# Kernel optimization log

Hardware: AMD Instinct MI355X
Metric: run time of the kernel (lower is better)

## Reference

```python
import jax, jax.numpy as jnp
import numpy as np

HEADS = 8
DIM_HEAD = 64
ROPE_THETA = 10000.0


def _rope(t):
    # t: [b, h, n, d]; interleaved-pair rotation as in rotary-embedding-torch
    n, d = t.shape[-2], t.shape[-1]
    inv_freq = 1.0 / (ROPE_THETA ** (jnp.arange(0, d, 2, dtype=jnp.float32) / d))  # [d/2]
    freqs = jnp.arange(n, dtype=jnp.float32)[:, None] * inv_freq[None, :]  # [n, d/2]
    freqs = jnp.repeat(freqs, 2, axis=-1)  # [n, d], repeated per pair
    cos, sin = jnp.cos(freqs), jnp.sin(freqs)
    x1 = t[..., 0::2]
    x2 = t[..., 1::2]
    rot = jnp.stack((-x2, x1), axis=-1).reshape(t.shape)  # rotate_half
    return t * cos + rot * sin


def setup_inputs() -> dict:
    key = jax.random.key(0)
    k1, k2, k3, k4 = jax.random.split(key, 4)
    b, n, dim = 2, 2048, 512
    hidden = HEADS * DIM_HEAD
    x = jax.random.normal(k1, (b, n, dim), dtype=jnp.float32)
    pos_bias = jax.random.normal(k2, (HEADS, n, n), dtype=jnp.float32) * 0.02
    w_qkv = jax.random.normal(k3, (dim, 3 * hidden), dtype=jnp.float32) * (dim ** -0.5)
    w_out = jax.random.normal(k4, (hidden, dim), dtype=jnp.float32) * (hidden ** -0.5)
    return {"x": x, "pos_bias": pos_bias, "w_qkv": w_qkv, "w_out": w_out}


def reference(x, pos_bias, w_qkv, w_out):
    b, n, _ = x.shape
    qkv = x @ w_qkv  # [b, n, 3*hidden]
    q, k, v = jnp.split(qkv, 3, axis=-1)

    def to_heads(t):
        return t.reshape(b, n, HEADS, DIM_HEAD).transpose(0, 2, 1, 3)  # [b,h,n,d]

    q, k, v = map(to_heads, (q, k, v))
    k = _rope(k)
    q = _rope(q * (DIM_HEAD ** -0.5))
    sim = jnp.einsum('bhid,bhjd->bhij', q, k)  # [b,h,n,n]
    sim = sim + pos_bias  # broadcast over batch
    sim = sim - jax.lax.stop_gradient(jnp.max(sim, axis=-1, keepdims=True))
    attn = jax.nn.softmax(sim, axis=-1)
    out = jnp.einsum('bhij,bhjd->bhid', attn, v)
    out = out.transpose(0, 2, 1, 3).reshape(b, n, HEADS * DIM_HEAD)
    return out @ w_out
```

## Files before the change

kernel.cpp:

```cpp
#include <hip/hip_runtime.h>
#include <math.h>

#define SEQ 2048
#define NHEAD 8
#define HDIM 64
#define BATCH 2

typedef __attribute__((ext_vector_type(8))) short short8;
typedef __attribute__((ext_vector_type(4))) float f32x4;

__device__ __forceinline__ ushort f2bf(float f) {
    union { float f; unsigned u; } v; v.f = f;
    unsigned r = v.u + 0x7FFFu + ((v.u >> 16) & 1u);
    return (ushort)(r >> 16);
}

__device__ __forceinline__ f32x4 mfma16(short8 a, short8 b, f32x4 c) {
    return __builtin_amdgcn_mfma_f32_16x16x32_bf16(a, b, c, 0, 0, 0);
}

__device__ __forceinline__ void gld16(const void* g, void* l) {
    __builtin_amdgcn_global_load_lds(
        (const __attribute__((address_space(1))) unsigned int*)g,
        (__attribute__((address_space(3))) unsigned int*)l, 16, 0, 0);
}

__device__ __forceinline__ int swz(int col, int row) {
    return (col & ~63) | ((((col >> 3) ^ row) & 7) << 3) | (col & 7);
}
__device__ __forceinline__ int lswz(int cb, int row) {
    return (((cb >> 3) ^ row) & 7) << 3;
}

__global__ __launch_bounds__(256)
void prep(const float* __restrict__ x, const float* __restrict__ w_qkv,
          const float* __restrict__ w_out, ushort* __restrict__ xb,
          ushort* __restrict__ wqkvT, ushort* __restrict__ woutT)
{
    __shared__ ushort tile[64][66];
    const int blk = blockIdx.x, t = threadIdx.x;
    if (blk < 1024) {
        const int i = (blk * 256 + t) * 8;
        const int m = i >> 9, k = i & 511;
        float4 a = *(const float4*)&x[i];
        float4 b = *(const float4*)&x[i + 4];
        union { ushort us[8]; uint4 v; } pk;
        pk.us[0] = f2bf(a.x); pk.us[1] = f2bf(a.y); pk.us[2] = f2bf(a.z); pk.us[3] = f2bf(a.w);
        pk.us[4] = f2bf(b.x); pk.us[5] = f2bf(b.y); pk.us[6] = f2bf(b.z); pk.us[7] = f2bf(b.w);
        *(uint4*)&xb[(size_t)m * 512 + swz(k, m)] = pk.v;
        return;
    }
    const float* w; ushort* wT; int K, N, n0, k0;
    if (blk < 1216) { const int s = blk - 1024; w = w_qkv; wT = wqkvT; K = 512; N = 1536; n0 = (s % 24) * 64; k0 = (s / 24) * 64; }
    else            { const int s = blk - 1216; w = w_out; wT = woutT; K = 512; N = 512;  n0 = (s % 8) * 64;  k0 = (s / 8) * 64; }
#pragma unroll
    for (int i = 0; i < 4; ++i) {
        const int slot = t + i * 256;
        const int r = slot >> 4, c4 = (slot & 15) * 4;
        float4 v = *(const float4*)&w[(size_t)(k0 + r) * N + n0 + c4];
        tile[c4 + 0][r] = f2bf(v.x);
        tile[c4 + 1][r] = f2bf(v.y);
        tile[c4 + 2][r] = f2bf(v.z);
        tile[c4 + 3][r] = f2bf(v.w);
    }
    __syncthreads();
    const int n = t >> 2, kc = (t & 3) * 16;
    union { ushort us[16]; uint4 v[2]; } o;
#pragma unroll
    for (int j = 0; j < 16; ++j) o.us[j] = tile[n][kc + j];
    const int ng = n0 + n;
    *(uint4*)&wT[(size_t)ng * K + swz(k0 + kc, ng)]     = o.v[0];
    *(uint4*)&wT[(size_t)ng * K + swz(k0 + kc + 8, ng)] = o.v[1];
}

__global__ __launch_bounds__(256)
void gemm_qkv_rope(const ushort* __restrict__ xb, const ushort* __restrict__ wT,
                   ushort* __restrict__ qb, ushort* __restrict__ kb,
                   ushort* __restrict__ vtb)
{
    __shared__ __align__(16) ushort As[2][64][64];
    __shared__ __align__(16) ushort Bs[2][128][64];
    const int t = threadIdx.x, lane = t & 63, w = t >> 6;
    const int quad = lane >> 4, l16 = lane & 15;
    const int m0 = blockIdx.y * 64, n0 = blockIdx.x * 128;
    const int mw = (w >> 1) * 32, nw = (w & 1) * 64;
    const int krow = lane >> 3, kcol = (lane & 7) * 8;
    f32x4 acc[2][4] = {};

    gld16(&xb[(size_t)(m0 + w * 8 + krow) * 512 + kcol],        &As[0][w * 8][0]);
    gld16(&xb[(size_t)(m0 + (w + 4) * 8 + krow) * 512 + kcol],  &As[0][(w + 4) * 8][0]);
#pragma unroll
    for (int jj = 0; jj < 4; ++jj)
        gld16(&wT[(size_t)(n0 + (w * 4 + jj) * 8 + krow) * 512 + kcol], &Bs[0][(w * 4 + jj) * 8][0]);
    __syncthreads();

    for (int k0 = 0; k0 < 512; k0 += 64) {
        const int cur = (k0 >> 6) & 1;
        if (k0 < 448) {
            gld16(&xb[(size_t)(m0 + w * 8 + krow) * 512 + k0 + 64 + kcol],        &As[cur ^ 1][w * 8][0]);
            gld16(&xb[(size_t)(m0 + (w + 4) * 8 + krow) * 512 + k0 + 64 + kcol],  &As[cur ^ 1][(w + 4) * 8][0]);
#pragma unroll
            for (int jj = 0; jj < 4; ++jj)
                gld16(&wT[(size_t)(n0 + (w * 4 + jj) * 8 + krow) * 512 + k0 + 64 + kcol], &Bs[cur ^ 1][(w * 4 + jj) * 8][0]);
        }
#pragma unroll
        for (int ks = 0; ks < 2; ++ks) {
            short8 a[2], b[4];
#pragma unroll
            for (int i = 0; i < 2; ++i) {
                const int row = mw + i * 16 + l16;
                a[i] = *(const short8*)&As[cur][row][lswz(ks * 32 + quad * 8, row)];
            }
#pragma unroll
            for (int j = 0; j < 4; ++j) {
                const int row = nw + j * 16 + l16;
                b[j] = *(const short8*)&Bs[cur][row][lswz(ks * 32 + quad * 8, row)];
            }
#pragma unroll
            for (int i = 0; i < 2; ++i)
#pragma unroll
                for (int j = 0; j < 4; ++j)
                    acc[i][j] = mfma16(a[i], b[j], acc[i][j]);
        }
        __syncthreads();
    }

    const int sec = (n0 + nw) >> 9;
    if (sec == 2) {
#pragma unroll
        for (int i = 0; i < 2; ++i) {
            const int m = m0 + mw + i * 16 + quad * 4;
            const int bidx = m >> 11, n = m & 2047;
#pragma unroll
            for (int j = 0; j < 4; ++j) {
                const int nc = n0 + nw + j * 16 + l16;
                const int d = nc & 63, h = (nc >> 6) & 7;
                ushort4 pk;
                pk.x = f2bf(acc[i][j][0]); pk.y = f2bf(acc[i][j][1]);
                pk.z = f2bf(acc[i][j][2]); pk.w = f2bf(acc[i][j][3]);
                *(ushort4*)&vtb[(((size_t)bidx * 8 + h) * 64 + d) * 2048 + swz(n, d)] = pk;
            }
        }
    } else {
        ushort* dst = (sec == 0) ? qb : kb;
        const float scale = (sec == 0) ? 0.125f : 1.0f;
#pragma unroll
        for (int j = 0; j < 4; ++j) {
            const int nc = n0 + nw + j * 16 + l16;
            const int d = nc & 63, h = (nc >> 6) & 7;
            const float inv = __expf(-(float)(d & ~1) * (9.2103403719761836f / 64.0f));
#pragma unroll
            for (int i = 0; i < 2; ++i)
#pragma unroll
            for (int r = 0; r < 4; ++r) {
                const int m = m0 + mw + i * 16 + quad * 4 + r;
                const int bidx = m >> 11, n = m & 2047;
                float sn, cs;
                __sincosf((float)n * inv, &sn, &cs);
                const float vacc = acc[i][j][r];
                const float partner = __shfl_xor(vacc, 1);
                const float rot = (d & 1) ? (vacc * cs + partner * sn)
                                          : (vacc * cs - partner * sn);
                const int dcol = (sec == 0) ? d : swz(d, n);
                dst[(((size_t)bidx * 8 + h) * 2048 + n) * 64 + dcol] = f2bf(rot * scale);
            }
        }
    }
}

__global__ __launch_bounds__(256)
void flash_attn_mfma(const ushort* __restrict__ qb, const ushort* __restrict__ kb,
                     const ushort* __restrict__ vtb, const float* __restrict__ bias,
                     ushort* __restrict__ ob)
{
    __shared__ __align__(16) ushort Ks[2][64][64];
    __shared__ __align__(16) ushort Vt[2][64][64];
    __shared__ __align__(16) float  Bl[2][64][64];
    __shared__ __align__(16) ushort Ps[4][16][72];
    const int t = threadIdx.x, lane = t & 63, w = t >> 6;
    const int quad = lane >> 4, l16 = lane & 15;
    const int q0 = blockIdx.x * 64, h = blockIdx.y, b = blockIdx.z;
    const size_t bh = (size_t)(b * NHEAD + h);
    const ushort* Q  = qb  + bh * SEQ * HDIM;
    const ushort* Kp = kb  + bh * SEQ * HDIM;
    const ushort* VT = vtb + bh * HDIM * SEQ;

    short8 qf[2];
    qf[0] = *(const short8*)&Q[(size_t)(q0 + w * 16 + l16) * HDIM + quad * 8];
    qf[1] = *(const short8*)&Q[(size_t)(q0 + w * 16 + l16) * HDIM + 32 + quad * 8];

    f32x4 oacc[4] = {};
    float lsum[4] = {};
    const int krow = lane >> 3, kcol = (lane & 7) * 8;
    const int brow = lane >> 4, bcol = (lane & 15) * 4;

    gld16(&Kp[(size_t)(w * 8 + krow) * HDIM + kcol],       &Ks[0][w * 8][0]);
    gld16(&Kp[(size_t)((w + 4) * 8 + krow) * HDIM + kcol], &Ks[0][(w + 4) * 8][0]);
    gld16(&VT[(size_t)(w * 8 + krow) * SEQ + kcol],        &Vt[0][w * 8][0]);
    gld16(&VT[(size_t)((w + 4) * 8 + krow) * SEQ + kcol],  &Vt[0][(w + 4) * 8][0]);
#pragma unroll
    for (int jj = 0; jj < 4; ++jj)
        gld16(&bias[((size_t)h * SEQ + q0 + (w * 4 + jj) * 4 + brow) * SEQ + bcol], &Bl[0][(w * 4 + jj) * 4][0]);
    __syncthreads();

    for (int it = 0; it < 32; ++it) {
        const int cur = it & 1;
        const int k0 = it * 64;
        if (it < 31) {
            const int kn = k0 + 64;
            gld16(&Kp[(size_t)(kn + w * 8 + krow) * HDIM + kcol],       &Ks[cur ^ 1][w * 8][0]);
            gld16(&Kp[(size_t)(kn + (w + 4) * 8 + krow) * HDIM + kcol], &Ks[cur ^ 1][(w + 4) * 8][0]);
            gld16(&VT[(size_t)(w * 8 + krow) * SEQ + kn + kcol],        &Vt[cur ^ 1][w * 8][0]);
            gld16(&VT[(size_t)((w + 4) * 8 + krow) * SEQ + kn + kcol],  &Vt[cur ^ 1][(w + 4) * 8][0]);
#pragma unroll
            for (int jj = 0; jj < 4; ++jj)
                gld16(&bias[((size_t)h * SEQ + q0 + (w * 4 + jj) * 4 + brow) * SEQ + kn + bcol], &Bl[cur ^ 1][(w * 4 + jj) * 4][0]);
        }

        f32x4 sacc[4] = {};
#pragma unroll
        for (int ks = 0; ks < 2; ++ks)
#pragma unroll
            for (int s = 0; s < 4; ++s) {
                const int row = s * 16 + l16;
                short8 kf = *(const short8*)&Ks[cur][row][lswz(ks * 32 + quad * 8, row)];
                sacc[s] = mfma16(qf[ks], kf, sacc[s]);
            }

#pragma unroll
        for (int r = 0; r < 4; ++r)
#pragma unroll
            for (int s = 0; s < 4; ++s) {
                const float p = __expf(sacc[s][r] + Bl[cur][w * 16 + quad * 4 + r][s * 16 + l16]);
                lsum[r] += p;
                Ps[w][quad * 4 + r][s * 16 + l16] = f2bf(p);
            }
        asm volatile("" ::: "memory");

#pragma unroll
        for (int ks = 0; ks < 2; ++ks) {
            short8 pf = *(const short8*)&Ps[w][l16][ks * 32 + quad * 8];
#pragma unroll
            for (int s = 0; s < 4; ++s) {
                const int row = s * 16 + l16;
                short8 vf = *(const short8*)&Vt[cur][row][lswz(ks * 32 + quad * 8, row)];
                oacc[s] = mfma16(pf, vf, oacc[s]);
            }
        }
        __syncthreads();
    }

#pragma unroll
    for (int r = 0; r < 4; ++r) {
        float rs = lsum[r];
        rs += __shfl_xor(rs, 1, 16);
        rs += __shfl_xor(rs, 2, 16);
        rs += __shfl_xor(rs, 4, 16);
        rs += __shfl_xor(rs, 8, 16);
        const float invl = 1.0f / rs;
        const int m = b * SEQ + q0 + w * 16 + quad * 4 + r;
#pragma unroll
        for (int s = 0; s < 4; ++s) {
            const int col = h * HDIM + s * 16 + l16;
            ob[(size_t)m * 512 + swz(col, m)] = f2bf(oacc[s][r] * invl);
        }
    }
}

__global__ __launch_bounds__(256)
void gemm_out(const ushort* __restrict__ Ab, const ushort* __restrict__ wT,
              float* __restrict__ C)
{
    __shared__ __align__(16) ushort As[2][64][64];
    __shared__ __align__(16) ushort Bs[2][64][64];
    const int t = threadIdx.x, lane = t & 63, w = t >> 6;
    const int quad = lane >> 4, l16 = lane & 15;
    const int m0 = blockIdx.y * 64, n0 = blockIdx.x * 64;
    const int mw = (w >> 1) * 32, nw = (w & 1) * 32;
    const int krow = lane >> 3, kcol = (lane & 7) * 8;
    f32x4 acc[2][2] = {};

    gld16(&Ab[(size_t)(m0 + w * 8 + krow) * 512 + kcol],       &As[0][w * 8][0]);
    gld16(&Ab[(size_t)(m0 + (w + 4) * 8 + krow) * 512 + kcol], &As[0][(w + 4) * 8][0]);
    gld16(&wT[(size_t)(n0 + w * 8 + krow) * 512 + kcol],       &Bs[0][w * 8][0]);
    gld16(&wT[(size_t)(n0 + (w + 4) * 8 + krow) * 512 + kcol], &Bs[0][(w + 4) * 8][0]);
    __syncthreads();

    for (int k0 = 0; k0 < 512; k0 += 64) {
        const int cur = (k0 >> 6) & 1;
        if (k0 < 448) {
            gld16(&Ab[(size_t)(m0 + w * 8 + krow) * 512 + k0 + 64 + kcol],       &As[cur ^ 1][w * 8][0]);
            gld16(&Ab[(size_t)(m0 + (w + 4) * 8 + krow) * 512 + k0 + 64 + kcol], &As[cur ^ 1][(w + 4) * 8][0]);
            gld16(&wT[(size_t)(n0 + w * 8 + krow) * 512 + k0 + 64 + kcol],       &Bs[cur ^ 1][w * 8][0]);
            gld16(&wT[(size_t)(n0 + (w + 4) * 8 + krow) * 512 + k0 + 64 + kcol], &Bs[cur ^ 1][(w + 4) * 8][0]);
        }
#pragma unroll
        for (int ks = 0; ks < 2; ++ks) {
            short8 a[2], b[2];
#pragma unroll
            for (int i = 0; i < 2; ++i) {
                const int row = mw + i * 16 + l16;
                a[i] = *(const short8*)&As[cur][row][lswz(ks * 32 + quad * 8, row)];
            }
#pragma unroll
            for (int j = 0; j < 2; ++j) {
                const int row = nw + j * 16 + l16;
                b[j] = *(const short8*)&Bs[cur][row][lswz(ks * 32 + quad * 8, row)];
            }
#pragma unroll
            for (int i = 0; i < 2; ++i)
#pragma unroll
                for (int j = 0; j < 2; ++j)
                    acc[i][j] = mfma16(a[i], b[j], acc[i][j]);
        }
        __syncthreads();
    }
#pragma unroll
    for (int i = 0; i < 2; ++i)
#pragma unroll
    for (int r = 0; r < 4; ++r) {
        const int m = m0 + mw + i * 16 + quad * 4 + r;
#pragma unroll
        for (int j = 0; j < 2; ++j)
            C[(size_t)m * 512 + n0 + nw + j * 16 + l16] = acc[i][j][r];
    }
}

extern "C" void kernel_launch(void* const* d_in, const int* in_sizes, int n_in,
                              void* d_out, int out_size, void* d_ws, size_t ws_size,
                              hipStream_t stream)
{
    const float* x        = (const float*)d_in[0];
    const float* pos_bias = (const float*)d_in[1];
    const float* w_qkv    = (const float*)d_in[2];
    const float* w_out    = (const float*)d_in[3];
    float* out = (float*)d_out;

    char* ws = (char*)d_ws;
    ushort* xb     = (ushort*)(ws);
    ushort* wqkvT  = (ushort*)(ws + 4194304);
    ushort* woutT  = (ushort*)(ws + 5767168);
    ushort* qb     = (ushort*)(ws + 6291456);
    ushort* kb     = (ushort*)(ws + 10485760);
    ushort* vtb    = (ushort*)(ws + 14680064);
    ushort* attnb  = (ushort*)(ws + 18874368);

    prep<<<1280, 256, 0, stream>>>(x, w_qkv, w_out, xb, wqkvT, woutT);
    gemm_qkv_rope<<<dim3(12, 64), 256, 0, stream>>>(xb, wqkvT, qb, kb, vtb);
    flash_attn_mfma<<<dim3(SEQ / 64, NHEAD, BATCH), 256, 0, stream>>>(qb, kb, vtb, pos_bias, attnb);
    gemm_out<<<dim3(8, 64), 256, 0, stream>>>(attnb, woutT, out);
}
```

Baseline: 258.2 us.

## Stage epilogue stores through LDS and prefetch bias into registers

The QKV GEMM epilogue for Q/K now writes rotated values into a per-wave LDS patch, then stores them as vectorized 8-byte chunks instead of scattered 2-byte stores. The attention kernel drops the LDS bias buffer and prefetches the bias tile straight into a double-buffered register array, which cuts LDS use and the LDS round trip. The attention output is also staged through the Ps buffer so it can be written with vectorized stores. The cost is more register pressure from the bias array, which may lower occupancy. The LDS reuse relies on wave-local ordering, enforced only by compiler barriers.

```diff
diff --git a/kernel.cpp b/kernel.cpp
--- a/kernel.cpp
+++ b/kernel.cpp
@@ -126,6 +126,7 @@
     }
 
     const int sec = (n0 + nw) >> 9;
+    const int h = ((n0 + nw) >> 6) & 7;
     if (sec == 2) {
 #pragma unroll
         for (int i = 0; i < 2; ++i) {
@@ -133,8 +134,7 @@
             const int bidx = m >> 11, n = m & 2047;
 #pragma unroll
             for (int j = 0; j < 4; ++j) {
-                const int nc = n0 + nw + j * 16 + l16;
-                const int d = nc & 63, h = (nc >> 6) & 7;
+                const int d = j * 16 + l16;
                 ushort4 pk;
                 pk.x = f2bf(acc[i][j][0]); pk.y = f2bf(acc[i][j][1]);
                 pk.z = f2bf(acc[i][j][2]); pk.w = f2bf(acc[i][j][3]);
@@ -144,26 +144,38 @@
     } else {
         ushort* dst = (sec == 0) ? qb : kb;
         const float scale = (sec == 0) ? 0.125f : 1.0f;
+        ushort* patch = (ushort*)Bs + (size_t)w * 32 * 68;
 #pragma unroll
         for (int j = 0; j < 4; ++j) {
-            const int nc = n0 + nw + j * 16 + l16;
-            const int d = nc & 63, h = (nc >> 6) & 7;
+            const int d = j * 16 + l16;
             const float inv = __expf(-(float)(d & ~1) * (9.2103403719761836f / 64.0f));
 #pragma unroll
             for (int i = 0; i < 2; ++i)
 #pragma unroll
             for (int r = 0; r < 4; ++r) {
                 const int m = m0 + mw + i * 16 + quad * 4 + r;
-                const int bidx = m >> 11, n = m & 2047;
+                const int n = m & 2047;
                 float sn, cs;
                 __sincosf((float)n * inv, &sn, &cs);
                 const float vacc = acc[i][j][r];
                 const float partner = __shfl_xor(vacc, 1);
                 const float rot = (d & 1) ? (vacc * cs + partner * sn)
                                           : (vacc * cs - partner * sn);
-                const int dcol = (sec == 0) ? d : swz(d, n);
-                dst[(((size_t)bidx * 8 + h) * 2048 + n) * 64 + dcol] = f2bf(rot * scale);
-            }
+                patch[(i * 16 + quad * 4 + r) * 68 + d] = f2bf(rot * scale);
+            }
+        }
+        asm volatile("" ::: "memory");
+        const int rl = lane >> 1;
+        const int mg = m0 + mw + rl;
+        const int bidx = mg >> 11, n = mg & 2047;
+        ushort* drow = &dst[(((size_t)bidx * 8 + h) * 2048 + n) * 64];
+#pragma unroll
+        for (int c = 0; c < 8; ++c) {
+            const int d4 = ((lane & 1) + 2 * c) * 4;
+            ushort4 v = *(const ushort4*)&patch[rl * 68 + d4];
+            const int dcol = (sec == 0) ? d4
+                : ((((d4 >> 3) ^ n) & 7) << 3) | (d4 & 7);
+            *(ushort4*)&drow[dcol] = v;
         }
     }
 }
@@ -175,7 +187,6 @@
 {
     __shared__ __align__(16) ushort Ks[2][64][64];
     __shared__ __align__(16) ushort Vt[2][64][64];
-    __shared__ __align__(16) float  Bl[2][64][64];
     __shared__ __align__(16) ushort Ps[4][16][72];
     const int t = threadIdx.x, lane = t & 63, w = t >> 6;
     const int quad = lane >> 4, l16 = lane & 15;
@@ -192,15 +203,18 @@
     f32x4 oacc[4] = {};
     float lsum[4] = {};
     const int krow = lane >> 3, kcol = (lane & 7) * 8;
-    const int brow = lane >> 4, bcol = (lane & 15) * 4;
+    const float* bias_base = bias + ((size_t)h * SEQ + q0 + w * 16 + quad * 4) * SEQ;
 
     gld16(&Kp[(size_t)(w * 8 + krow) * HDIM + kcol],       &Ks[0][w * 8][0]);
     gld16(&Kp[(size_t)((w + 4) * 8 + krow) * HDIM + kcol], &Ks[0][(w + 4) * 8][0]);
     gld16(&VT[(size_t)(w * 8 + krow) * SEQ + kcol],        &Vt[0][w * 8][0]);
     gld16(&VT[(size_t)((w + 4) * 8 + krow) * SEQ + kcol],  &Vt[0][(w + 4) * 8][0]);
-#pragma unroll
-    for (int jj = 0; jj < 4; ++jj)
-        gld16(&bias[((size_t)h * SEQ + q0 + (w * 4 + jj) * 4 + brow) * SEQ + bcol], &Bl[0][(w * 4 + jj) * 4][0]);
+    float bv[2][4][4];
+#pragma unroll
+    for (int r = 0; r < 4; ++r)
+#pragma unroll
+        for (int s = 0; s < 4; ++s)
+            bv[0][r][s] = bias_base[(size_t)r * SEQ + s * 16 + l16];
     __syncthreads();
 
     for (int it = 0; it < 32; ++it) {
@@ -213,8 +227,10 @@
             gld16(&VT[(size_t)(w * 8 + krow) * SEQ + kn + kcol],        &Vt[cur ^ 1][w * 8][0]);
             gld16(&VT[(size_t)((w + 4) * 8 + krow) * SEQ + kn + kcol],  &Vt[cur ^ 1][(w + 4) * 8][0]);
 #pragma unroll
-            for (int jj = 0; jj < 4; ++jj)
-                gld16(&bias[((size_t)h * SEQ + q0 + (w * 4 + jj) * 4 + brow) * SEQ + kn + bcol], &Bl[cur ^ 1][(w * 4 + jj) * 4][0]);
+            for (int r = 0; r < 4; ++r)
+#pragma unroll
+                for (int s = 0; s < 4; ++s)
+                    bv[cur ^ 1][r][s] = bias_base[(size_t)r * SEQ + kn + s * 16 + l16];
         }
 
         f32x4 sacc[4] = {};
@@ -231,7 +247,7 @@
         for (int r = 0; r < 4; ++r)
 #pragma unroll
             for (int s = 0; s < 4; ++s) {
-                const float p = __expf(sacc[s][r] + Bl[cur][w * 16 + quad * 4 + r][s * 16 + l16]);
+                const float p = __expf(sacc[s][r] + bv[cur][r][s]);
                 lsum[r] += p;
                 Ps[w][quad * 4 + r][s * 16 + l16] = f2bf(p);
             }
@@ -250,6 +266,7 @@
         __syncthreads();
     }
 
+    float invl[4];
 #pragma unroll
     for (int r = 0; r < 4; ++r) {
         float rs = lsum[r];
@@ -257,13 +274,22 @@
         rs += __shfl_xor(rs, 2, 16);
         rs += __shfl_xor(rs, 4, 16);
         rs += __shfl_xor(rs, 8, 16);
-        const float invl = 1.0f / rs;
-        const int m = b * SEQ + q0 + w * 16 + quad * 4 + r;
-#pragma unroll
-        for (int s = 0; s < 4; ++s) {
-            const int col = h * HDIM + s * 16 + l16;
-            ob[(size_t)m * 512 + swz(col, m)] = f2bf(oacc[s][r] * invl);
-        }
+        invl[r] = 1.0f / rs;
+    }
+#pragma unroll
+    for (int r = 0; r < 4; ++r)
+#pragma unroll
+        for (int s = 0; s < 4; ++s)
+            Ps[w][quad * 4 + r][s * 16 + l16] = f2bf(oacc[s][r] * invl[r]);
+    asm volatile("" ::: "memory");
+    const int rl = lane >> 2;
+    const int m = b * SEQ + q0 + w * 16 + rl;
+#pragma unroll
+    for (int c = 0; c < 4; ++c) {
+        const int d4 = ((lane & 3) + 4 * c) * 4;
+        ushort4 v = *(const ushort4*)&Ps[w][rl][d4];
+        const int col = h * HDIM + ((((d4 >> 3) ^ m) & 7) << 3) + (d4 & 7);
+        *(ushort4*)&ob[(size_t)m * 512 + col] = v;
     }
 }
 
```

New measurement: 349.7 us. 35.4% more time.
